# Optimization experiments

Hardware: AMD Instinct MI355X
Metric: run time of the kernel (lower is better)

## Reference

```python
import jax, jax.numpy as jnp
import numpy as np

N_THETA = 180  # matches init kwarg n_theta


def setup_inputs() -> dict:
    key = jax.random.key(0)
    image = jax.random.normal(key, (2, 1, 256, 256), dtype=jnp.float32)
    return {"image": image}


def _radon_forward(image):
    # image: [B, 1, W, W]
    B, _, W, _ = image.shape
    # circle=False: pad to the diagonal so rotation never clips content
    diag = 2.0 ** 0.5 * W
    pad = int(np.ceil(diag - W))
    S = int(np.ceil(diag))                    # padded square size (363 for W=256)
    new_center = (W + pad) // 2
    pad_before = new_center - W // 2
    pad_after = pad - pad_before
    img = jnp.pad(image[:, 0], ((0, 0), (pad_before, pad_after), (pad_before, pad_after)))  # [B,S,S]

    thetas = jnp.deg2rad(jnp.linspace(0.0, 180.0, N_THETA))
    cos_a = jnp.cos(thetas)[:, None, None]    # [A,1,1]
    sin_a = jnp.sin(thetas)[:, None, None]

    # torch affine_grid(align_corners=True): base grid in [-1,1] inclusive
    base = jnp.linspace(-1.0, 1.0, S)
    y = base[:, None]                          # height index i
    x = base[None, :]                          # width index j
    # theta = [[c, s, 0], [-s, c, 0]] -> sample coords per angle, [A,S,S]
    gx = cos_a * x + sin_a * y
    gy = -sin_a * x + cos_a * y

    # grid_sample align_corners=True: pixel coord = (g+1)/2*(S-1)
    px = (gx + 1.0) * 0.5 * (S - 1)
    py = (gy + 1.0) * 0.5 * (S - 1)
    x0 = jnp.floor(px).astype(jnp.int32); x1 = x0 + 1
    y0 = jnp.floor(py).astype(jnp.int32); y1 = y0 + 1
    wx1 = px - x0; wx0 = 1.0 - wx1
    wy1 = py - y0; wy0 = 1.0 - wy1

    def fetch(yi, xi):
        # zeros padding: out-of-range taps contribute 0
        valid = ((yi >= 0) & (yi < S) & (xi >= 0) & (xi < S)).astype(img.dtype)
        yc = jnp.clip(yi, 0, S - 1)
        xc = jnp.clip(xi, 0, S - 1)
        return img[:, yc, xc] * valid[None]    # [B,A,S,S]

    sampled = (fetch(y0, x0) * (wy0 * wx0)[None]
               + fetch(y0, x1) * (wy0 * wx1)[None]
               + fetch(y1, x0) * (wy1 * wx0)[None]
               + fetch(y1, x1) * (wy1 * wx1)[None])   # [B,A,S,S]

    sino = sampled.sum(axis=2)                 # sum over height -> [B,A,S]
    # torch: stack along dim=2 then permute(0,1,3,2) -> [B,1,S,A]
    return jnp.transpose(sino, (0, 2, 1))[:, None]


def reference(image):
    return _radon_forward(image)
```

## Files before the change

kernel.cpp:

```cpp
#include <hip/hip_runtime.h>
#include <math.h>
#include <stdint.h>


#define SS 363
#define WW 256
#define NT 180
#define AP 9
#define QDIM (WW + 2 * AP)
#define QCNT (QDIM * QDIM)
#define NTILE 46
#define NRANGE (NT * NTILE)
#define NBQ ((QCNT + 255) / 256)
#define NBR ((NRANGE + 255) / 256)

#define QOFF 0
#define SCOFF (QCNT * 16)
#define RGOFF (SCOFF + ((NT * 8 + 15) & ~15))
#define WSNEED (RGOFF + NRANGE * 4)

typedef _Float16 h8 __attribute__((ext_vector_type(8)));
typedef __fp16  h2 __attribute__((ext_vector_type(2)));

#if defined(__has_builtin)
#if __has_builtin(__builtin_amdgcn_fdot2) && __has_builtin(__builtin_amdgcn_cvt_pkrtz)
#define USE_DOT2 1
#endif
#endif

__global__ __launch_bounds__(256) void radon_prep(const float* __restrict__ img,
                                                  char* __restrict__ ws) {
    h8* __restrict__ q = (h8*)(ws + QOFF);
    if (blockIdx.x < NBQ) {
        const int idx = blockIdx.x * 256 + threadIdx.x;
        if (idx >= QCNT) return;
        const int iy = idx / QDIM;
        const int ix = idx - iy * QDIM;
        const int y0 = iy - AP, x0 = ix - AP;
        const bool xin0 = ((unsigned)x0 < (unsigned)WW);
        const bool xin1 = ((unsigned)(x0 + 1) < (unsigned)WW);
        const bool yin0 = ((unsigned)y0 < (unsigned)WW);
        const bool yin1 = ((unsigned)(y0 + 1) < (unsigned)WW);
        h8 o;
        #pragma unroll
        for (int b = 0; b < 2; ++b) {
            const float* __restrict__ im = img + b * WW * WW;
            float v00 = 0.f, v01 = 0.f, v10 = 0.f, v11 = 0.f;
            if (yin0) {
                const float* r0 = im + y0 * WW;
                if (xin0) v00 = r0[x0];
                if (xin1) v01 = r0[x0 + 1];
            }
            if (yin1) {
                const float* r1 = im + (y0 + 1) * WW;
                if (xin0) v10 = r1[x0];
                if (xin1) v11 = r1[x0 + 1];
            }
            o[4 * b + 0] = (_Float16)v00;
            o[4 * b + 1] = (_Float16)v01;
            o[4 * b + 2] = (_Float16)v10;
            o[4 * b + 3] = (_Float16)v11;
        }
        q[idx] = o;
    } else {
        const int ridx = (blockIdx.x - NBQ) * 256 + threadIdx.x;
        if (ridx >= NRANGE) return;
        const int t    = ridx / NTILE;
        const int tile = ridx - t * NTILE;
        float sv, cv;
        sincosf((float)t * 0.017551608191455498f, &sv, &cv);
        if (tile == 0) ((float2*)(ws + SCOFF))[t] = make_float2(sv, cv);
        int Ulo = SS;
        int Uhi = -1;
        #pragma unroll
        for (int cl = 0; cl < 8; ++cl) {
            const int c = tile * 8 + cl;
            const float x   = fmaf((float)c, 0.0055248618784530386f, -1.0f);
            const float px0 = fmaf(fmaf(cv, x, -sv), 181.0f, 128.0f);
            const float py0 = fmaf(fmaf(-sv, x, -cv), 181.0f, 128.0f);
            float rlo = 0.0f, rhi = 362.0f;
            if (fabsf(sv) > 1e-8f) {
                const float ra = (-1.0f - px0) / sv, rb = (256.0f - px0) / sv;
                rlo = fmaxf(rlo, fminf(ra, rb)); rhi = fminf(rhi, fmaxf(ra, rb));
            } else if (px0 <= -1.0f || px0 >= 256.0f) rhi = -2.0f;
            if (fabsf(cv) > 1e-8f) {
                const float ra = (-1.0f - py0) / cv, rb = (256.0f - py0) / cv;
                rlo = fmaxf(rlo, fminf(ra, rb)); rhi = fminf(rhi, fmaxf(ra, rb));
            } else if (py0 <= -1.0f || py0 >= 256.0f) rhi = -2.0f;
            const int Rlo = min(max(0, (int)floorf(rlo) - 1), SS);
            const int Rhi = max(min(SS - 1, (int)ceilf(rhi) + 1), -1);
            Ulo = min(Ulo, Rlo);
            Uhi = max(Uhi, Rhi);
        }
        ((int*)(ws + RGOFF))[ridx] =
            ((int)(unsigned short)(short)Ulo) | ((int)(short)Uhi << 16);
    }
}

__global__ __launch_bounds__(256) void radon_main(const char* __restrict__ ws,
                                                  float* __restrict__ out) {
    const int tid = threadIdx.x;
    const int w   = tid >> 6;
    const int l   = tid & 63;
    const int cl  = l & 7;
    const int rl  = l >> 3;
    const int tile = blockIdx.x;
    const int t    = blockIdx.y;

    const float2 sc = ((const float2*)(ws + SCOFF))[t];
    const float sv = sc.x, cv = sc.y;
    const int rr = ((const int*)(ws + RGOFF))[t * NTILE + tile];
    const int Rlo = (int)(short)(rr & 0xffff);
    const int Rhi = rr >> 16;

    const int c = tile * 8 + cl;
    const float x   = fmaf((float)c, 0.0055248618784530386f, -1.0f);
    const float px0 = fmaf(fmaf(cv, x, -sv), 181.0f, 128.0f);
    const float py0 = fmaf(fmaf(-sv, x, -cv), 181.0f, 128.0f);

    const uint4* __restrict__ qb = (const uint4*)(ws + QOFF);
    const int base_off = AP * QDIM + AP;
    float acc0 = 0.0f, acc1 = 0.0f;
    #pragma unroll 2
    for (int r = Rlo + rl + 8 * w; r <= Rhi; r += 32) {
        const float rf = (float)r;
        const float px = fmaf(rf, sv, px0);
        const float py = fmaf(rf, cv, py0);
        const float fx = floorf(px), fy = floorf(py);
        const float wx1 = px - fx, wy1 = py - fy;
        const float wx0 = 1.0f - wx1, wy0 = 1.0f - wy1;
        const int idx = (int)fmaf(fy, (float)QDIM, fx) + base_off;
        const uint4 u = qb[idx];
#ifdef USE_DOT2
        const h2 wlo = __builtin_amdgcn_cvt_pkrtz(wy0 * wx0, wy0 * wx1);
        const h2 whi = __builtin_amdgcn_cvt_pkrtz(wy1 * wx0, wy1 * wx1);
        acc0 = __builtin_amdgcn_fdot2(wlo, __builtin_bit_cast(h2, u.x), acc0, false);
        acc0 = __builtin_amdgcn_fdot2(whi, __builtin_bit_cast(h2, u.y), acc0, false);
        acc1 = __builtin_amdgcn_fdot2(wlo, __builtin_bit_cast(h2, u.z), acc1, false);
        acc1 = __builtin_amdgcn_fdot2(whi, __builtin_bit_cast(h2, u.w), acc1, false);
#else
        const h2 v01 = __builtin_bit_cast(h2, u.x);
        const h2 v23 = __builtin_bit_cast(h2, u.y);
        const h2 v45 = __builtin_bit_cast(h2, u.z);
        const h2 v67 = __builtin_bit_cast(h2, u.w);
        const float top0 = fmaf(wx0, (float)v01[0], wx1 * (float)v01[1]);
        const float bot0 = fmaf(wx0, (float)v23[0], wx1 * (float)v23[1]);
        acc0 = fmaf(wy0, top0, acc0);
        acc0 = fmaf(wy1, bot0, acc0);
        const float top1 = fmaf(wx0, (float)v45[0], wx1 * (float)v45[1]);
        const float bot1 = fmaf(wx0, (float)v67[0], wx1 * (float)v67[1]);
        acc1 = fmaf(wy0, top1, acc1);
        acc1 = fmaf(wy1, bot1, acc1);
#endif
    }
    acc0 += __shfl_xor(acc0, 8, 64);
    acc0 += __shfl_xor(acc0, 16, 64);
    acc0 += __shfl_xor(acc0, 32, 64);
    acc1 += __shfl_xor(acc1, 8, 64);
    acc1 += __shfl_xor(acc1, 16, 64);
    acc1 += __shfl_xor(acc1, 32, 64);

    __shared__ float p0[4][8], p1[4][8];
    if (l < 8) { p0[w][l] = acc0; p1[w][l] = acc1; }
    __syncthreads();
    if (tid < 8) {
        const int cc = tile * 8 + tid;
        if (cc < SS) {
            out[(0 * SS + cc) * NT + t] =
                p0[0][tid] + p0[1][tid] + p0[2][tid] + p0[3][tid];
            out[(1 * SS + cc) * NT + t] =
                p1[0][tid] + p1[1][tid] + p1[2][tid] + p1[3][tid];
        }
    }
}

__global__ __launch_bounds__(256) void radon_fwd_fb(const float* __restrict__ img,
                                                    float* __restrict__ out) {
    const int tid = threadIdx.x;
    const int w = tid >> 6, l = tid & 63, cl = l & 7, rl = l >> 3;
    const int c0 = blockIdx.x * 8, c = c0 + cl, t = blockIdx.y, b = blockIdx.z;
    float sv, cv;
    sincosf((float)t * 0.017551608191455498f, &sv, &cv);
    const float x   = fmaf((float)c, 0.0055248618784530386f, -1.0f);
    const float px0 = fmaf(fmaf(cv, x, -sv), 181.0f, 128.0f);
    const float py0 = fmaf(fmaf(-sv, x, -cv), 181.0f, 128.0f);
    float rlo = 0.0f, rhi = 362.0f;
    if (fabsf(sv) > 1e-8f) {
        const float ra = (-1.0f - px0) / sv, rb = (256.0f - px0) / sv;
        rlo = fmaxf(rlo, fminf(ra, rb)); rhi = fminf(rhi, fmaxf(ra, rb));
    } else if (px0 <= -1.0f || px0 >= 256.0f) rhi = -2.0f;
    if (fabsf(cv) > 1e-8f) {
        const float ra = (-1.0f - py0) / cv, rb = (256.0f - py0) / cv;
        rlo = fmaxf(rlo, fminf(ra, rb)); rhi = fminf(rhi, fmaxf(ra, rb));
    } else if (py0 <= -1.0f || py0 >= 256.0f) rhi = -2.0f;
    int Rlo = max(0, (int)floorf(rlo) - 1);
    int Rhi = min(SS - 1, (int)ceilf(rhi) + 1);
    #pragma unroll
    for (int o = 1; o <= 4; o <<= 1) {
        Rlo = min(Rlo, __shfl_xor(Rlo, o, 64));
        Rhi = max(Rhi, __shfl_xor(Rhi, o, 64));
    }
    const float* __restrict__ imgb = img + b * (WW * WW);
    float acc = 0.0f;
    for (int r = Rlo + 8 * w + rl; r <= Rhi; r += 32) {
        const float rf = (float)r;
        const float px = fmaf(rf, sv, px0), py = fmaf(rf, cv, py0);
        const float fx = floorf(px), fy = floorf(py);
        float wx1 = px - fx, wy1 = py - fy;
        float wx0 = 1.0f - wx1, wy0 = 1.0f - wy1;
        const int x0 = (int)fx, y0 = (int)fy, x1 = x0 + 1, y1 = y0 + 1;
        wx0 *= ((unsigned)x0 < (unsigned)WW) ? 1.0f : 0.0f;
        wx1 *= ((unsigned)x1 < (unsigned)WW) ? 1.0f : 0.0f;
        wy0 *= ((unsigned)y0 < (unsigned)WW) ? 1.0f : 0.0f;
        wy1 *= ((unsigned)y1 < (unsigned)WW) ? 1.0f : 0.0f;
        const int xc0 = min(max(x0, 0), WW - 1), xc1 = min(max(x1, 0), WW - 1);
        const int yc0 = min(max(y0, 0), WW - 1), yc1 = min(max(y1, 0), WW - 1);
        const float* r0p = imgb + yc0 * WW;
        const float* r1p = imgb + yc1 * WW;
        const float top = fmaf(wx0, r0p[xc0], wx1 * r0p[xc1]);
        const float bot = fmaf(wx0, r1p[xc0], wx1 * r1p[xc1]);
        acc = fmaf(wy0, top, acc);
        acc = fmaf(wy1, bot, acc);
    }
    acc += __shfl_xor(acc, 8, 64);
    acc += __shfl_xor(acc, 16, 64);
    acc += __shfl_xor(acc, 32, 64);
    __shared__ float part[4][8];
    if (l < 8) part[w][l] = acc;
    __syncthreads();
    if (tid < 8) {
        const int cc = c0 + tid;
        if (cc < SS)
            out[(b * SS + cc) * NT + t] =
                part[0][tid] + part[1][tid] + part[2][tid] + part[3][tid];
    }
}

extern "C" void kernel_launch(void* const* d_in, const int* in_sizes, int n_in,
                              void* d_out, int out_size, void* d_ws, size_t ws_size,
                              hipStream_t stream) {
    (void)in_sizes; (void)n_in; (void)out_size;
    const float* img = (const float*)d_in[0];
    float* out = (float*)d_out;
    if (ws_size >= (size_t)WSNEED) {
        char* ws = (char*)d_ws;
        hipLaunchKernelGGL(radon_prep, dim3(NBQ + NBR), dim3(256), 0,
                           stream, img, ws);
        dim3 grid(NTILE, NT, 1);
        hipLaunchKernelGGL(radon_main, grid, dim3(256), 0, stream, ws, out);
    } else {
        dim3 grid((SS + 7) / 8, NT, 2);
        hipLaunchKernelGGL(radon_fwd_fb, grid, dim3(256), 0, stream, img, out);
    }
}
```

Measured before the change: 71.91 us.

## Fuse prep and main kernels into one cooperative kernel with grid sync

Merges the precompute kernel (fp16 quad packing and per-tile row ranges) and the main sampling kernel into one cooperative launch of 1024 persistent blocks. The blocks do the prep work, meet at a grid-wide barrier, then loop over the (angle, tile) pairs. This removes one kernel launch and the gap between the two kernels. The cost is a grid sync, an extra __syncthreads per pair, and a fixed block count that spreads 8280 pairs unevenly across blocks. It falls back to the two-kernel path if the cooperative launch fails.

```diff
diff --git a/kernel.cpp b/kernel.cpp
--- a/kernel.cpp
+++ b/kernel.cpp
@@ -1,7 +1,10 @@
 #include <hip/hip_runtime.h>
+#include <hip/hip_cooperative_groups.h>
 #include <math.h>
 #include <stdint.h>
 
+
+namespace cg = cooperative_groups;
 
 #define SS 363
 #define WW 256
@@ -28,88 +31,83 @@
 #endif
 #endif
 
-__global__ __launch_bounds__(256) void radon_prep(const float* __restrict__ img,
-                                                  char* __restrict__ ws) {
-    h8* __restrict__ q = (h8*)(ws + QOFF);
-    if (blockIdx.x < NBQ) {
-        const int idx = blockIdx.x * 256 + threadIdx.x;
-        if (idx >= QCNT) return;
-        const int iy = idx / QDIM;
-        const int ix = idx - iy * QDIM;
-        const int y0 = iy - AP, x0 = ix - AP;
-        const bool xin0 = ((unsigned)x0 < (unsigned)WW);
-        const bool xin1 = ((unsigned)(x0 + 1) < (unsigned)WW);
-        const bool yin0 = ((unsigned)y0 < (unsigned)WW);
-        const bool yin1 = ((unsigned)(y0 + 1) < (unsigned)WW);
-        h8 o;
-        #pragma unroll
-        for (int b = 0; b < 2; ++b) {
-            const float* __restrict__ im = img + b * WW * WW;
-            float v00 = 0.f, v01 = 0.f, v10 = 0.f, v11 = 0.f;
-            if (yin0) {
-                const float* r0 = im + y0 * WW;
-                if (xin0) v00 = r0[x0];
-                if (xin1) v01 = r0[x0 + 1];
-            }
-            if (yin1) {
-                const float* r1 = im + (y0 + 1) * WW;
-                if (xin0) v10 = r1[x0];
-                if (xin1) v11 = r1[x0 + 1];
-            }
-            o[4 * b + 0] = (_Float16)v00;
-            o[4 * b + 1] = (_Float16)v01;
-            o[4 * b + 2] = (_Float16)v10;
-            o[4 * b + 3] = (_Float16)v11;
-        }
-        q[idx] = o;
-    } else {
-        const int ridx = (blockIdx.x - NBQ) * 256 + threadIdx.x;
-        if (ridx >= NRANGE) return;
-        const int t    = ridx / NTILE;
-        const int tile = ridx - t * NTILE;
-        float sv, cv;
-        sincosf((float)t * 0.017551608191455498f, &sv, &cv);
-        if (tile == 0) ((float2*)(ws + SCOFF))[t] = make_float2(sv, cv);
-        int Ulo = SS;
-        int Uhi = -1;
-        #pragma unroll
-        for (int cl = 0; cl < 8; ++cl) {
-            const int c = tile * 8 + cl;
-            const float x   = fmaf((float)c, 0.0055248618784530386f, -1.0f);
-            const float px0 = fmaf(fmaf(cv, x, -sv), 181.0f, 128.0f);
-            const float py0 = fmaf(fmaf(-sv, x, -cv), 181.0f, 128.0f);
-            float rlo = 0.0f, rhi = 362.0f;
-            if (fabsf(sv) > 1e-8f) {
-                const float ra = (-1.0f - px0) / sv, rb = (256.0f - px0) / sv;
-                rlo = fmaxf(rlo, fminf(ra, rb)); rhi = fminf(rhi, fmaxf(ra, rb));
-            } else if (px0 <= -1.0f || px0 >= 256.0f) rhi = -2.0f;
-            if (fabsf(cv) > 1e-8f) {
-                const float ra = (-1.0f - py0) / cv, rb = (256.0f - py0) / cv;
-                rlo = fmaxf(rlo, fminf(ra, rb)); rhi = fminf(rhi, fmaxf(ra, rb));
-            } else if (py0 <= -1.0f || py0 >= 256.0f) rhi = -2.0f;
-            const int Rlo = min(max(0, (int)floorf(rlo) - 1), SS);
-            const int Rhi = max(min(SS - 1, (int)ceilf(rhi) + 1), -1);
-            Ulo = min(Ulo, Rlo);
-            Uhi = max(Uhi, Rhi);
-        }
-        ((int*)(ws + RGOFF))[ridx] =
-            ((int)(unsigned short)(short)Ulo) | ((int)(short)Uhi << 16);
-    }
-}
-
-__global__ __launch_bounds__(256) void radon_main(const char* __restrict__ ws,
-                                                  float* __restrict__ out) {
-    const int tid = threadIdx.x;
-    const int w   = tid >> 6;
-    const int l   = tid & 63;
-    const int cl  = l & 7;
-    const int rl  = l >> 3;
-    const int tile = blockIdx.x;
-    const int t    = blockIdx.y;
+__device__ __forceinline__ void pack_quad(const float* __restrict__ img,
+                                          h8* __restrict__ q, int idx) {
+    const int iy = idx / QDIM;
+    const int ix = idx - iy * QDIM;
+    const int y0 = iy - AP, x0 = ix - AP;
+    const bool xin0 = ((unsigned)x0 < (unsigned)WW);
+    const bool xin1 = ((unsigned)(x0 + 1) < (unsigned)WW);
+    const bool yin0 = ((unsigned)y0 < (unsigned)WW);
+    const bool yin1 = ((unsigned)(y0 + 1) < (unsigned)WW);
+    h8 o;
+    #pragma unroll
+    for (int b = 0; b < 2; ++b) {
+        const float* __restrict__ im = img + b * WW * WW;
+        float v00 = 0.f, v01 = 0.f, v10 = 0.f, v11 = 0.f;
+        if (yin0) {
+            const float* r0 = im + y0 * WW;
+            if (xin0) v00 = r0[x0];
+            if (xin1) v01 = r0[x0 + 1];
+        }
+        if (yin1) {
+            const float* r1 = im + (y0 + 1) * WW;
+            if (xin0) v10 = r1[x0];
+            if (xin1) v11 = r1[x0 + 1];
+        }
+        o[4 * b + 0] = (_Float16)v00;
+        o[4 * b + 1] = (_Float16)v01;
+        o[4 * b + 2] = (_Float16)v10;
+        o[4 * b + 3] = (_Float16)v11;
+    }
+    q[idx] = o;
+}
+
+__device__ __forceinline__ void compute_range(char* __restrict__ ws, int ridx) {
+    const int t    = ridx / NTILE;
+    const int tile = ridx - t * NTILE;
+    float sv, cv;
+    sincosf((float)t * 0.017551608191455498f, &sv, &cv);
+    if (tile == 0) ((float2*)(ws + SCOFF))[t] = make_float2(sv, cv);
+    int Ulo = SS, Uhi = -1;
+    #pragma unroll
+    for (int cl = 0; cl < 8; ++cl) {
+        const int c = tile * 8 + cl;
+        const float x   = fmaf((float)c, 0.0055248618784530386f, -1.0f);
+        const float px0 = fmaf(fmaf(cv, x, -sv), 181.0f, 128.0f);
+        const float py0 = fmaf(fmaf(-sv, x, -cv), 181.0f, 128.0f);
+        float rlo = 0.0f, rhi = 362.0f;
+        if (fabsf(sv) > 1e-8f) {
+            const float ra = (-1.0f - px0) / sv, rb = (256.0f - px0) / sv;
+            rlo = fmaxf(rlo, fminf(ra, rb)); rhi = fminf(rhi, fmaxf(ra, rb));
+        } else if (px0 <= -1.0f || px0 >= 256.0f) rhi = -2.0f;
+        if (fabsf(cv) > 1e-8f) {
+            const float ra = (-1.0f - py0) / cv, rb = (256.0f - py0) / cv;
+            rlo = fmaxf(rlo, fminf(ra, rb)); rhi = fminf(rhi, fmaxf(ra, rb));
+        } else if (py0 <= -1.0f || py0 >= 256.0f) rhi = -2.0f;
+        const int Rlo = min(max(0, (int)floorf(rlo) - 1), SS);
+        const int Rhi = max(min(SS - 1, (int)ceilf(rhi) + 1), -1);
+        Ulo = min(Ulo, Rlo);
+        Uhi = max(Uhi, Rhi);
+    }
+    ((int*)(ws + RGOFF))[ridx] =
+        ((int)(unsigned short)(short)Ulo) | ((int)(short)Uhi << 16);
+}
+
+__device__ __forceinline__ void do_pair(const char* __restrict__ ws,
+                                        float* __restrict__ out,
+                                        int pair, int tid,
+                                        float (*p0)[8], float (*p1)[8]) {
+    const int w  = tid >> 6;
+    const int l  = tid & 63;
+    const int cl = l & 7;
+    const int rl = l >> 3;
+    const int t    = pair / NTILE;
+    const int tile = pair - t * NTILE;
 
     const float2 sc = ((const float2*)(ws + SCOFF))[t];
     const float sv = sc.x, cv = sc.y;
-    const int rr = ((const int*)(ws + RGOFF))[t * NTILE + tile];
+    const int rr = ((const int*)(ws + RGOFF))[pair];
     const int Rlo = (int)(short)(rr & 0xffff);
     const int Rhi = rr >> 16;
 
@@ -160,7 +158,6 @@
     acc1 += __shfl_xor(acc1, 16, 64);
     acc1 += __shfl_xor(acc1, 32, 64);
 
-    __shared__ float p0[4][8], p1[4][8];
     if (l < 8) { p0[w][l] = acc0; p1[w][l] = acc1; }
     __syncthreads();
     if (tid < 8) {
@@ -172,6 +169,44 @@
                 p1[0][tid] + p1[1][tid] + p1[2][tid] + p1[3][tid];
         }
     }
+    __syncthreads();
+}
+
+#define FUSED_BLOCKS 1024
+
+__global__ __launch_bounds__(256, 4) void radon_fused(const float* __restrict__ img,
+                                                      char* __restrict__ ws,
+                                                      float* __restrict__ out) {
+    const int tid  = threadIdx.x;
+    const int gidx = blockIdx.x * 256 + tid;
+    if (gidx < QCNT) {
+        pack_quad(img, (h8*)(ws + QOFF), gidx);
+    } else if (gidx < QCNT + NRANGE) {
+        compute_range(ws, gidx - QCNT);
+    }
+    cg::this_grid().sync();
+    __shared__ float p0[4][8], p1[4][8];
+    for (int pair = blockIdx.x; pair < NRANGE; pair += FUSED_BLOCKS)
+        do_pair(ws, out, pair, tid, p0, p1);
+}
+
+__global__ __launch_bounds__(256) void radon_prep(const float* __restrict__ img,
+                                                  char* __restrict__ ws) {
+    if (blockIdx.x < NBQ) {
+        const int idx = blockIdx.x * 256 + threadIdx.x;
+        if (idx >= QCNT) return;
+        pack_quad(img, (h8*)(ws + QOFF), idx);
+    } else {
+        const int ridx = (blockIdx.x - NBQ) * 256 + threadIdx.x;
+        if (ridx >= NRANGE) return;
+        compute_range(ws, ridx);
+    }
+}
+
+__global__ __launch_bounds__(256) void radon_main(const char* __restrict__ ws,
+                                                  float* __restrict__ out) {
+    __shared__ float p0[4][8], p1[4][8];
+    do_pair(ws, out, blockIdx.y * NTILE + blockIdx.x, threadIdx.x, p0, p1);
 }
 
 __global__ __launch_bounds__(256) void radon_fwd_fb(const float* __restrict__ img,
@@ -244,10 +279,16 @@
     float* out = (float*)d_out;
     if (ws_size >= (size_t)WSNEED) {
         char* ws = (char*)d_ws;
-        hipLaunchKernelGGL(radon_prep, dim3(NBQ + NBR), dim3(256), 0,
-                           stream, img, ws);
-        dim3 grid(NTILE, NT, 1);
-        hipLaunchKernelGGL(radon_main, grid, dim3(256), 0, stream, ws, out);
+        void* args[3] = {(void*)&img, (void*)&ws, (void*)&out};
+        hipError_t e = hipLaunchCooperativeKernel((void*)radon_fused,
+                                                  dim3(FUSED_BLOCKS), dim3(256),
+                                                  args, 0, stream);
+        if (e != hipSuccess) {
+            hipLaunchKernelGGL(radon_prep, dim3(NBQ + NBR), dim3(256), 0,
+                               stream, img, ws);
+            hipLaunchKernelGGL(radon_main, dim3(NTILE, NT, 1), dim3(256), 0,
+                               stream, ws, out);
+        }
     } else {
         dim3 grid((SS + 7) / 8, NT, 2);
         hipLaunchKernelGGL(radon_fwd_fb, grid, dim3(256), 0, stream, img, out);
```

Measured after the change: 156.8 us. 2.18x slower.
